# Performance work log

Hardware: AMD Instinct MI355X
Metric: run time of the kernel (lower is better)

Reference implementation:

```python
import jax, jax.numpy as jnp
import numpy as np

N = 131072
F_DIM = 128
HID = 256
POL = 512
EPS = 1e-5


def _lin(key, fan_in, fan_out):
    k1, k2 = jax.random.split(key)
    s = 1.0 / np.sqrt(fan_in)
    W = jax.random.uniform(k1, (fan_in, fan_out), jnp.float32, -s, s)
    b = jax.random.uniform(k2, (fan_out,), jnp.float32, -s, s)
    return W, b


def setup_inputs() -> dict:
    key = jax.random.key(0)
    ks = jax.random.split(key, 12)
    observation = jax.random.normal(ks[0], (N, F_DIM), jnp.float32)
    mask = jnp.ones((N, 1), jnp.float32)
    # dense_to_sparse(eye(N)) -> pure self-loop edge list
    ar = jnp.arange(N, dtype=jnp.int32)
    edge_index = jnp.stack([ar, ar])  # [2, N]
    W1, b1 = _lin(ks[1], F_DIM, HID)
    Wg, bg = _lin(ks[2], HID, HID)     # GCNConv weight/bias
    ln_w = jnp.ones((HID,), jnp.float32)
    ln_b = jnp.zeros((HID,), jnp.float32)
    Wgate, bgate = _lin(ks[3], HID, 1)
    Wd, bd = _lin(ks[4], HID, HID)
    Wp1, bp1 = _lin(ks[5], HID, POL)
    Wp2, bp2 = _lin(ks[6], POL, POL)
    Wv, bv = _lin(ks[7], POL, 1)
    return dict(observation=observation, mask=mask, edge_index=edge_index,
                W1=W1, b1=b1, Wg=Wg, bg=bg, ln_w=ln_w, ln_b=ln_b,
                Wgate=Wgate, bgate=bgate, Wd=Wd, bd=bd,
                Wp1=Wp1, bp1=bp1, Wp2=Wp2, bp2=bp2, Wv=Wv, bv=bv)


def reference(observation, mask, edge_index, W1, b1, Wg, bg, ln_w, ln_b,
              Wgate, bgate, Wd, bd, Wp1, bp1, Wp2, bp2, Wv, bv):
    n = observation.shape[0]
    # encoder_1 + relu
    X = jax.nn.relu(observation @ W1 + b1)  # [N,256]

    # GCNConv(256,256): add self-loops, symmetric norm, gather/scatter
    ar = jnp.arange(n, dtype=edge_index.dtype)
    ei = jnp.concatenate([edge_index, jnp.stack([ar, ar])], axis=1)  # [2,E+N]
    row, col = ei[0], ei[1]
    Xw = X @ Wg
    deg = jax.ops.segment_sum(jnp.ones(ei.shape[1], X.dtype), col, num_segments=n)
    dinv = jnp.where(deg > 0, jax.lax.rsqrt(deg), 0.0)
    norm = dinv[row] * dinv[col]
    msg = Xw[row] * norm[:, None]
    Xg = jax.ops.segment_sum(msg, col, num_segments=n) + bg
    Xg = jax.nn.relu(Xg)

    # PyG LayerNorm, mode='graph' (batch=None): global mean/std over all elements
    mu = Xg.mean()
    sd = jnp.sqrt(jnp.mean((Xg - mu) ** 2))  # std, unbiased=False
    Xn = (Xg - mu) / (sd + EPS) * ln_w + ln_b

    # AttentionalAggregation with sigmoid gate -> [1,256]
    gate = jax.nn.sigmoid(Xn @ Wgate + bgate)  # [N,1]
    pooled = jnp.sum(gate * Xn, axis=0, keepdims=True)

    h = jax.nn.relu(pooled @ Wd + bd)
    h = jax.nn.relu(h @ Wp1 + bp1)
    h = jax.nn.relu(h @ Wp2 + bp2)
    value = h @ Wv + bv  # [1,1]
    return value * mask  # broadcast -> [N,1]
```

## Files before the change

### kernel.cpp

```cpp
#include <hip/hip_runtime.h>

#define NROWS 131072
#define EPSV 1e-5f

typedef __attribute__((ext_vector_type(8))) short short8;
typedef __attribute__((ext_vector_type(4))) short bfx4;
typedef __attribute__((ext_vector_type(4))) float floatx4;

__device__ __forceinline__ short f2bf(float f){
  unsigned u = __builtin_bit_cast(unsigned, f);
  return (short)((u + 0x8000u) >> 16);
}
__device__ __forceinline__ float bf2f(unsigned h){
  unsigned u = h << 16;
  return __builtin_bit_cast(float, u);
}

__device__ __forceinline__ int XIDX(int row, int col){
  return row*256 + ((((col >> 3) ^ (row & 31))) << 3) + (col & 7);
}

__global__ __launch_bounds__(256) void prep_kernel(
    const float* __restrict__ W1, const float* __restrict__ Wg,
    const float* __restrict__ lnw, const float* __restrict__ lnb,
    const float* __restrict__ Wgate,
    short* __restrict__ W1s, short* __restrict__ Wgs,
    float* __restrict__ u, float* accum)
{
  const int b = blockIdx.x, tid = threadIdx.x;
  if (b < 16){
    int idx = b*256 + tid;
    int lane = idx & 63, rg = idx >> 6;
    int ctg = rg & 15, kt = rg >> 4;
    int kb = kt*32 + (lane>>4)*8;
    int c  = ctg*16 + (lane&15);
    short8 t;
    #pragma unroll
    for (int j=0;j<8;j++) t[j] = f2bf(W1[(kb+j)*256 + c]);
    *(short8*)(W1s + idx*8) = t;
  } else if (b < 48){
    int idx = (b-16)*256 + tid;
    int lane = idx & 63, rg = idx >> 6;
    int ctg = rg & 15, kt = rg >> 4;
    int kb = kt*32 + (lane>>4)*8;
    int c  = ctg*16 + (lane&15);
    short8 t;
    #pragma unroll
    for (int j=0;j<8;j++) t[j] = f2bf(Wg[(kb+j)*256 + c]);
    *(short8*)(Wgs + idx*8) = t;
  } else {
    __shared__ float red[8];
    float uv = lnw[tid] * Wgate[tid];
    float lv = lnb[tid] * Wgate[tid];
    u[tid] = uv;
    float a = uv, c = lv;
    #pragma unroll
    for (int off=32; off; off >>= 1){
      a += __shfl_down(a, off);
      c += __shfl_down(c, off);
    }
    const int w = tid >> 6, l = tid & 63;
    if (l == 0){ red[w] = a; red[4+w] = c; }
    __syncthreads();
    if (tid == 0){
      accum[4] = red[0]+red[1]+red[2]+red[3];
      accum[5] = red[4]+red[5]+red[6]+red[7];
    }
  }
}

__global__ __launch_bounds__(256, 3) void gemm12_kernel(
    const float* __restrict__ obs, const float* __restrict__ b1,
    const float* __restrict__ bg,
    const short* __restrict__ W1s, const short* __restrict__ Wgs,
    const float* __restrict__ u,
    short* __restrict__ XgT, float* __restrict__ d, float* __restrict__ pS)
{
  __shared__ short Xs[64*256];
  float* dacc = (float*)Xs;
  short* As = Xs;
  const int tid = threadIdx.x;
  const int w = tid >> 6, l = tid & 63, q = l >> 4, lm = l & 15;
  const long R = (long)blockIdx.x * 64;

  short8 bc[4], bn[4];
  float bias1[4];
  #pragma unroll
  for (int ct=0; ct<4; ct++){
    bc[ct] = *(const short8*)(W1s + (((w*4+ct))*64 + l)*8);
    bias1[ct] = b1[w*64 + ct*16 + lm];
  }

  #pragma unroll
  for (int rt=0; rt<4; rt++){
    const float* ap = obs + (R + rt*16 + lm)*128 + w*32 + q*8;
    floatx4 f0 = *(const floatx4*)ap;
    floatx4 f1 = *(const floatx4*)(ap + 4);
    short8 t;
    t[0]=f2bf(f0[0]); t[1]=f2bf(f0[1]); t[2]=f2bf(f0[2]); t[3]=f2bf(f0[3]);
    t[4]=f2bf(f1[0]); t[5]=f2bf(f1[1]); t[6]=f2bf(f1[2]); t[7]=f2bf(f1[3]);
    *(short8*)(As + ((w*4 + rt)*64 + l)*8) = t;
  }
  __syncthreads();

  floatx4 acc[4][4];
  #pragma unroll
  for (int ct=0; ct<4; ct++){
    floatx4 bi = {bias1[ct], bias1[ct], bias1[ct], bias1[ct]};
    #pragma unroll
    for (int rt=0; rt<4; rt++) acc[rt][ct] = bi;
  }

  short8 ac[4], an[4];
  #pragma unroll
  for (int rt=0; rt<4; rt++)
    ac[rt] = *(const short8*)(As + ((0*4 + rt)*64 + l)*8);
  #pragma unroll
  for (int kt=0; kt<4; kt++){
    if (kt < 3){
      #pragma unroll
      for (int ct=0; ct<4; ct++)
        bn[ct] = *(const short8*)(W1s + (((kt+1)*16 + (w*4+ct))*64 + l)*8);
      #pragma unroll
      for (int rt=0; rt<4; rt++)
        an[rt] = *(const short8*)(As + (((kt+1)*4 + rt)*64 + l)*8);
    }
    #pragma unroll
    for (int ct=0; ct<4; ct++)
      #pragma unroll
      for (int rt=0; rt<4; rt++)
        acc[rt][ct] = __builtin_amdgcn_mfma_f32_16x16x32_bf16(ac[rt], bc[ct], acc[rt][ct], 0,0,0);
    if (kt < 3){
      #pragma unroll
      for (int i=0;i<4;i++){ bc[i]=bn[i]; ac[i]=an[i]; }
    }
  }

  float bias2[4], uc[4];
  #pragma unroll
  for (int ct=0; ct<4; ct++){
    bc[ct] = *(const short8*)(Wgs + (((w*4+ct))*64 + l)*8);
    bias2[ct] = bg[w*64 + ct*16 + lm];
    uc[ct]    = u [w*64 + ct*16 + lm];
  }

  __syncthreads();

  #pragma unroll
  for (int ct=0; ct<4; ct++){
    const int col = w*64 + ct*16 + lm;
    #pragma unroll
    for (int rt=0; rt<4; rt++)
      #pragma unroll
      for (int r=0;r<4;r++)
        Xs[XIDX(rt*16 + q*4 + r, col)] = f2bf(fmaxf(acc[rt][ct][r], 0.f));
  }
  __syncthreads();

  #pragma unroll
  for (int ct=0; ct<4; ct++){
    floatx4 bi = {bias2[ct], bias2[ct], bias2[ct], bias2[ct]};
    #pragma unroll
    for (int rt=0; rt<4; rt++) acc[rt][ct] = bi;
  }
  #pragma unroll
  for (int rt=0; rt<4; rt++)
    ac[rt] = *(const short8*)(Xs + XIDX(rt*16 + lm, 0*32 + q*8));
  #pragma unroll
  for (int kt=0; kt<8; kt++){
    if (kt < 7){
      #pragma unroll
      for (int ct=0; ct<4; ct++)
        bn[ct] = *(const short8*)(Wgs + (((kt+1)*16 + (w*4+ct))*64 + l)*8);
      #pragma unroll
      for (int rt=0; rt<4; rt++)
        an[rt] = *(const short8*)(Xs + XIDX(rt*16 + lm, (kt+1)*32 + q*8));
    }
    #pragma unroll
    for (int ct=0; ct<4; ct++)
      #pragma unroll
      for (int rt=0; rt<4; rt++)
        acc[rt][ct] = __builtin_amdgcn_mfma_f32_16x16x32_bf16(ac[rt], bc[ct], acc[rt][ct], 0,0,0);
    if (kt < 7){
      #pragma unroll
      for (int i=0;i<4;i++){ bc[i]=bn[i]; ac[i]=an[i]; }
    }
  }
  __syncthreads();

  float s1 = 0.f, s2 = 0.f;
  float dp[16];
  #pragma unroll
  for (int i=0;i<16;i++) dp[i] = 0.f;
  #pragma unroll
  for (int ct=0; ct<4; ct++){
    const int col = w*64 + ct*16 + lm;
    const float uv = uc[ct];
    #pragma unroll
    for (int rt=0; rt<4; rt++){
      float v0 = fmaxf(acc[rt][ct][0], 0.f);
      float v1 = fmaxf(acc[rt][ct][1], 0.f);
      float v2 = fmaxf(acc[rt][ct][2], 0.f);
      float v3 = fmaxf(acc[rt][ct][3], 0.f);
      s1 += (v0+v1)+(v2+v3);
      s2 += v0*v0 + v1*v1 + v2*v2 + v3*v3;
      dp[rt*4+0] += v0*uv; dp[rt*4+1] += v1*uv;
      dp[rt*4+2] += v2*uv; dp[rt*4+3] += v3*uv;
      bfx4 pk = {f2bf(v0), f2bf(v1), f2bf(v2), f2bf(v3)};
      *(bfx4*)(XgT + (long)col*NROWS + R + rt*16 + q*4) = pk;
    }
  }
  #pragma unroll
  for (int rt=0; rt<4; rt++)
    #pragma unroll
    for (int r=0; r<4; r++)
      dacc[(w*64 + rt*16 + q*4 + r)*17 + lm] = dp[rt*4+r];

  #pragma unroll
  for (int off=32; off; off >>= 1){
    s1 += __shfl_down(s1, off);
    s2 += __shfl_down(s2, off);
  }
  if (l == 0){
    pS[blockIdx.x*4 + w] = s1;
    pS[8192 + blockIdx.x*4 + w] = s2;
  }
  __syncthreads();

  {
    const int row = tid >> 2, g = tid & 3;
    float s = 0.f;
    #pragma unroll
    for (int wv=0; wv<4; wv++)
      #pragma unroll
      for (int j=0; j<4; j++)
        s += dacc[(wv*64 + row)*17 + g*4 + j];
    s += __shfl_xor(s, 1);
    s += __shfl_xor(s, 2);
    if (g == 0) d[R + row] = s;
  }
}

__global__ __launch_bounds__(256) void stats_kernel(
    const float* __restrict__ pS, const float* __restrict__ bgate,
    float* __restrict__ accum)
{
  __shared__ float red[8];
  const int tid = threadIdx.x, w = tid >> 6, l = tid & 63;
  float a = 0.f, b = 0.f;
  #pragma unroll
  for (int i=0;i<32;i++){
    a += pS[tid + 256*i];
    b += pS[8192 + tid + 256*i];
  }
  #pragma unroll
  for (int off=32; off; off >>= 1){
    a += __shfl_down(a, off);
    b += __shfl_down(b, off);
  }
  if (l == 0){ red[w] = a; red[4+w] = b; }
  __syncthreads();
  if (tid == 0){
    const float NE = (float)NROWS * 256.f;
    const float S1 = red[0]+red[1]+red[2]+red[3];
    const float S2 = red[4]+red[5]+red[6]+red[7];
    const float mu = S1 / NE;
    float var = S2 / NE - mu*mu;
    var = var > 0.f ? var : 0.f;
    const float inv = 1.f / (sqrtf(var) + EPSV);
    accum[0] = inv;
    accum[1] = -inv*mu*accum[4] + accum[5] + bgate[0];
    accum[2] = mu;
  }
}

__global__ __launch_bounds__(256) void pool_kernel(
    const short* __restrict__ XgT, const float* __restrict__ dvec,
    const float* __restrict__ accum,
    float* __restrict__ gxPart, float* __restrict__ gsPart)
{
  __shared__ float spj[4][8];
  __shared__ float sgs[4];
  const int tid = threadIdx.x, w = tid >> 6, l = tid & 63;
  const float inv = accum[0];
  const float gc  = accum[1];

  const int rs = blockIdx.x >> 5, cg = blockIdx.x & 31, c0 = cg*8;
  float p[8];
  #pragma unroll
  for (int j=0;j<8;j++) p[j] = 0.f;
  float gs = 0.f;

  #pragma unroll
  for (int it=0; it<2; it++){
    const int r0 = rs*4096 + it*2048 + tid*8;
    floatx4 dv0 = *(const floatx4*)(dvec + r0);
    floatx4 dv1 = *(const floatx4*)(dvec + r0 + 4);
    float g[8];
    g[0] = 1.f/(1.f + __expf(-(inv*dv0[0] + gc)));
    g[1] = 1.f/(1.f + __expf(-(inv*dv0[1] + gc)));
    g[2] = 1.f/(1.f + __expf(-(inv*dv0[2] + gc)));
    g[3] = 1.f/(1.f + __expf(-(inv*dv0[3] + gc)));
    g[4] = 1.f/(1.f + __expf(-(inv*dv1[0] + gc)));
    g[5] = 1.f/(1.f + __expf(-(inv*dv1[1] + gc)));
    g[6] = 1.f/(1.f + __expf(-(inv*dv1[2] + gc)));
    g[7] = 1.f/(1.f + __expf(-(inv*dv1[3] + gc)));
    gs += ((g[0]+g[1])+(g[2]+g[3])) + ((g[4]+g[5])+(g[6]+g[7]));
    #pragma unroll
    for (int j=0;j<8;j++){
      short8 xv = *(const short8*)(XgT + (long)(c0+j)*NROWS + r0);
      float s = 0.f;
      #pragma unroll
      for (int k=0;k<8;k++) s += g[k]*bf2f((unsigned short)xv[k]);
      p[j] += s;
    }
  }
  #pragma unroll
  for (int j=0;j<8;j++)
    #pragma unroll
    for (int off=32; off; off >>= 1) p[j] += __shfl_down(p[j], off);
  #pragma unroll
  for (int off=32; off; off >>= 1) gs += __shfl_down(gs, off);
  if (l == 0){
    #pragma unroll
    for (int j=0;j<8;j++) spj[w][j] = p[j];
    sgs[w] = gs;
  }
  __syncthreads();
  if (tid < 8)
    gxPart[rs*256 + c0 + tid] = spj[0][tid]+spj[1][tid]+spj[2][tid]+spj[3][tid];
  if (cg == 0 && tid == 8)
    gsPart[rs] = sgs[0]+sgs[1]+sgs[2]+sgs[3];
}

__global__ __launch_bounds__(256) void mlp1_kernel(
    const float* __restrict__ lnw, const float* __restrict__ lnb,
    const float* __restrict__ Wd,  const float* __restrict__ bd,
    const float* __restrict__ accum, const float* __restrict__ gxPart,
    const float* __restrict__ gsPart, float* __restrict__ h1)
{
  __shared__ float xa[256];
  __shared__ float redG;
  __shared__ float sp[4][64];
  const int tid = threadIdx.x, w = tid >> 6, l = tid & 63;
  const float inv = accum[0];
  const float mu  = accum[2];

  if (w == 0){
    float gg = (l < 32) ? gsPart[l] : 0.f;
    #pragma unroll
    for (int off=32; off; off >>= 1) gg += __shfl_down(gg, off);
    if (l == 0) redG = gg;
  }
  __syncthreads();
  const float G = redG;

  {
    float sgx = 0.f;
    #pragma unroll
    for (int s=0;s<32;s++) sgx += gxPart[s*256 + tid];
    const float lw = lnw[tid];
    xa[tid] = inv*lw*sgx + (lnb[tid] - mu*inv*lw)*G;
  }
  __syncthreads();

  const int j = blockIdx.x*64 + l;
  const int k0 = w*64;
  const float* wp = Wd + (long)k0*256 + j;
  float p0=0.f,p1=0.f,p2=0.f,p3=0.f;
  #pragma unroll
  for (int k=0; k<64; k+=4){
    p0 += xa[k0+k  ] * wp[(k  )*256];
    p1 += xa[k0+k+1] * wp[(k+1)*256];
    p2 += xa[k0+k+2] * wp[(k+2)*256];
    p3 += xa[k0+k+3] * wp[(k+3)*256];
  }
  sp[w][l] = (p0+p1)+(p2+p3);
  __syncthreads();
  if (w == 0)
    h1[j] = fmaxf(sp[0][l]+sp[1][l]+sp[2][l]+sp[3][l] + bd[j], 0.f);
}

__global__ __launch_bounds__(256) void mlp_mid(
    const float* __restrict__ W, const float* __restrict__ bias,
    const float* __restrict__ x, float* __restrict__ y,
    const int inDim, const int outDim)
{
  __shared__ float sp[4][64];
  const int l = threadIdx.x & 63, w = threadIdx.x >> 6;
  const int j = blockIdx.x*64 + l;
  const int kq = inDim >> 2, k0 = w*kq;
  const float* wp = W + (long)k0*outDim + j;
  float p0=0.f,p1=0.f,p2=0.f,p3=0.f;
  for (int k=0; k<kq; k+=4){
    p0 += x[k0+k  ] * wp[(long)(k  )*outDim];
    p1 += x[k0+k+1] * wp[(long)(k+1)*outDim];
    p2 += x[k0+k+2] * wp[(long)(k+2)*outDim];
    p3 += x[k0+k+3] * wp[(long)(k+3)*outDim];
  }
  sp[w][l] = (p0+p1)+(p2+p3);
  __syncthreads();
  if (w == 0)
    y[j] = fmaxf(sp[0][l]+sp[1][l]+sp[2][l]+sp[3][l] + bias[j], 0.f);
}

__global__ __launch_bounds__(256) void bcast_kernel(
    const float* __restrict__ h3, const float* __restrict__ Wv,
    const float* __restrict__ bv, const float* __restrict__ mask,
    float* __restrict__ out)
{
  __shared__ float red[4];
  const int tid = threadIdx.x, w = tid >> 6, l = tid & 63;
  float p = h3[tid]*Wv[tid] + h3[tid+256]*Wv[tid+256];
  #pragma unroll
  for (int off=32; off; off >>= 1) p += __shfl_down(p, off);
  if (l == 0) red[w] = p;
  __syncthreads();
  const float value = red[0]+red[1]+red[2]+red[3] + bv[0];

  const long i = (long)blockIdx.x*256 + tid;
  floatx4 m = *(const floatx4*)(mask + i*4);
  floatx4 o = {m[0]*value, m[1]*value, m[2]*value, m[3]*value};
  *(floatx4*)(out + i*4) = o;
}

extern "C" void kernel_launch(void* const* d_in, const int* in_sizes, int n_in,
                              void* d_out, int out_size, void* d_ws, size_t ws_size,
                              hipStream_t stream)
{
  const float* obs   = (const float*)d_in[0];
  const float* mask  = (const float*)d_in[1];
  const float* W1    = (const float*)d_in[3];
  const float* b1    = (const float*)d_in[4];
  const float* Wg    = (const float*)d_in[5];
  const float* bg    = (const float*)d_in[6];
  const float* lnw   = (const float*)d_in[7];
  const float* lnb   = (const float*)d_in[8];
  const float* Wgate = (const float*)d_in[9];
  const float* bgate = (const float*)d_in[10];
  const float* Wd    = (const float*)d_in[11];
  const float* bd    = (const float*)d_in[12];
  const float* Wp1   = (const float*)d_in[13];
  const float* bp1   = (const float*)d_in[14];
  const float* Wp2   = (const float*)d_in[15];
  const float* bp2   = (const float*)d_in[16];
  const float* Wv    = (const float*)d_in[17];
  const float* bv    = (const float*)d_in[18];
  float* out = (float*)d_out;

  char* wsb = (char*)d_ws;
  short* XgT   = (short*)(wsb);
  short* W1s   = (short*)(wsb + 67108864);
  short* Wgs   = (short*)(wsb + 67174400);
  float* u     = (float*)(wsb + 67305472);
  float* dvec  = (float*)(wsb + 67306496);
  float* pS    = (float*)(wsb + 67830784);
  float* gxP   = (float*)(wsb + 67896320);
  float* gsP   = (float*)(wsb + 67929088);
  float* accum = (float*)(wsb + 67930112);
  float* h1    = (float*)(wsb + 67931136);
  float* h2    = (float*)(wsb + 67932160);
  float* h3    = (float*)(wsb + 67934208);

  prep_kernel<<<49, 256, 0, stream>>>(W1, Wg, lnw, lnb, Wgate, W1s, Wgs, u, accum);
  gemm12_kernel<<<2048, 256, 0, stream>>>(obs, b1, bg, W1s, Wgs, u, XgT, dvec, pS);
  stats_kernel<<<1, 256, 0, stream>>>(pS, bgate, accum);
  pool_kernel<<<1024, 256, 0, stream>>>(XgT, dvec, accum, gxP, gsP);
  mlp1_kernel<<<4, 256, 0, stream>>>(lnw, lnb, Wd, bd, accum, gxP, gsP, h1);
  mlp_mid<<<8, 256, 0, stream>>>(Wp1, bp1, h1, h2, 256, 512);
  mlp_mid<<<8, 256, 0, stream>>>(Wp2, bp2, h2, h3, 512, 512);
  bcast_kernel<<<128, 256, 0, stream>>>(h3, Wv, bv, mask, out);
}
```

Measured before the change: 221.5 us.

## Fuse stats into GEMM via last-block counter and merge MLP tail kernels

The separate stats kernel is removed. The last gemm12 block to finish, found with an atomic counter and threadfence, now reduces the partial sums and writes the normalization constants. The four small MLP and broadcast kernels are merged into one tail kernel of 16 blocks, and each block recomputes the whole MLP before writing its slice of the output. This removes several launch and inter-kernel gaps, at the cost of redundant MLP work in each block and a serialized reduction at the end of the GEMM.

```diff
diff --git a/kernel.cpp b/kernel.cpp
--- a/kernel.cpp
+++ b/kernel.cpp
@@ -25,7 +25,7 @@
     const float* __restrict__ lnw, const float* __restrict__ lnb,
     const float* __restrict__ Wgate,
     short* __restrict__ W1s, short* __restrict__ Wgs,
-    float* __restrict__ u, float* accum)
+    float* __restrict__ u, float* accum, unsigned* __restrict__ counter)
 {
   const int b = blockIdx.x, tid = threadIdx.x;
   if (b < 16){
@@ -65,6 +65,7 @@
     if (tid == 0){
       accum[4] = red[0]+red[1]+red[2]+red[3];
       accum[5] = red[4]+red[5]+red[6]+red[7];
+      counter[0] = 0u;
     }
   }
 }
@@ -73,10 +74,12 @@
     const float* __restrict__ obs, const float* __restrict__ b1,
     const float* __restrict__ bg,
     const short* __restrict__ W1s, const short* __restrict__ Wgs,
-    const float* __restrict__ u,
-    short* __restrict__ XgT, float* __restrict__ d, float* __restrict__ pS)
+    const float* __restrict__ u, const float* __restrict__ bgate,
+    short* __restrict__ XgT, float* __restrict__ d, float* __restrict__ pS,
+    float* __restrict__ accum, unsigned* __restrict__ counter)
 {
   __shared__ short Xs[64*256];
+  __shared__ unsigned tick;
   float* dacc = (float*)Xs;
   short* As = Xs;
   const int tid = threadIdx.x;
@@ -239,38 +242,38 @@
     s += __shfl_xor(s, 2);
     if (g == 0) d[R + row] = s;
   }
-}
-
-__global__ __launch_bounds__(256) void stats_kernel(
-    const float* __restrict__ pS, const float* __restrict__ bgate,
-    float* __restrict__ accum)
-{
-  __shared__ float red[8];
-  const int tid = threadIdx.x, w = tid >> 6, l = tid & 63;
-  float a = 0.f, b = 0.f;
-  #pragma unroll
-  for (int i=0;i<32;i++){
-    a += pS[tid + 256*i];
-    b += pS[8192 + tid + 256*i];
-  }
-  #pragma unroll
-  for (int off=32; off; off >>= 1){
-    a += __shfl_down(a, off);
-    b += __shfl_down(b, off);
-  }
-  if (l == 0){ red[w] = a; red[4+w] = b; }
-  __syncthreads();
-  if (tid == 0){
-    const float NE = (float)NROWS * 256.f;
-    const float S1 = red[0]+red[1]+red[2]+red[3];
-    const float S2 = red[4]+red[5]+red[6]+red[7];
-    const float mu = S1 / NE;
-    float var = S2 / NE - mu*mu;
-    var = var > 0.f ? var : 0.f;
-    const float inv = 1.f / (sqrtf(var) + EPSV);
-    accum[0] = inv;
-    accum[1] = -inv*mu*accum[4] + accum[5] + bgate[0];
-    accum[2] = mu;
+
+  __threadfence();
+  __syncthreads();
+  if (tid == 0) tick = atomicAdd(counter, 1u);
+  __syncthreads();
+  if (tick == 2047u){
+    __threadfence();
+    float a = 0.f, b = 0.f;
+    #pragma unroll
+    for (int i=0;i<32;i++){
+      a += pS[tid + 256*i];
+      b += pS[8192 + tid + 256*i];
+    }
+    #pragma unroll
+    for (int off=32; off; off >>= 1){
+      a += __shfl_down(a, off);
+      b += __shfl_down(b, off);
+    }
+    if (l == 0){ dacc[w] = a; dacc[4+w] = b; }
+    __syncthreads();
+    if (tid == 0){
+      const float NE = (float)NROWS * 256.f;
+      const float S1 = dacc[0]+dacc[1]+dacc[2]+dacc[3];
+      const float S2 = dacc[4]+dacc[5]+dacc[6]+dacc[7];
+      const float mu = S1 / NE;
+      float var = S2 / NE - mu*mu;
+      var = var > 0.f ? var : 0.f;
+      const float inv = 1.f / (sqrtf(var) + EPSV);
+      accum[0] = inv;
+      accum[1] = -inv*mu*accum[4] + accum[5] + bgate[0];
+      accum[2] = mu;
+    }
   }
 }
 
@@ -333,18 +336,22 @@
     gsPart[rs] = sgs[0]+sgs[1]+sgs[2]+sgs[3];
 }
 
-__global__ __launch_bounds__(256) void mlp1_kernel(
+__global__ __launch_bounds__(256) void tail_kernel(
     const float* __restrict__ lnw, const float* __restrict__ lnb,
     const float* __restrict__ Wd,  const float* __restrict__ bd,
+    const float* __restrict__ Wp1, const float* __restrict__ bp1,
+    const float* __restrict__ Wp2, const float* __restrict__ bp2,
+    const float* __restrict__ Wv,  const float* __restrict__ bv,
     const float* __restrict__ accum, const float* __restrict__ gxPart,
-    const float* __restrict__ gsPart, float* __restrict__ h1)
+    const float* __restrict__ gsPart, const float* __restrict__ mask,
+    float* __restrict__ out)
 {
-  __shared__ float xa[256];
+  __shared__ float xa[256], v1[256], v2[512], v3[512];
+  __shared__ float sp[2048];
+  __shared__ float redv[4];
   __shared__ float redG;
-  __shared__ float sp[4][64];
   const int tid = threadIdx.x, w = tid >> 6, l = tid & 63;
-  const float inv = accum[0];
-  const float mu  = accum[2];
+  const float inv = accum[0], mu = accum[2];
 
   if (w == 0){
     float gg = (l < 32) ? gsPart[l] : 0.f;
@@ -352,76 +359,96 @@
     for (int off=32; off; off >>= 1) gg += __shfl_down(gg, off);
     if (l == 0) redG = gg;
   }
-  __syncthreads();
-  const float G = redG;
-
-  {
-    float sgx = 0.f;
-    #pragma unroll
-    for (int s=0;s<32;s++) sgx += gxPart[s*256 + tid];
-    const float lw = lnw[tid];
+  float sgx = 0.f;
+  #pragma unroll
+  for (int s=0;s<32;s++) sgx += gxPart[s*256 + tid];
+  __syncthreads();
+  {
+    const float G = redG, lw = lnw[tid];
     xa[tid] = inv*lw*sgx + (lnb[tid] - mu*inv*lw)*G;
   }
   __syncthreads();
 
-  const int j = blockIdx.x*64 + l;
-  const int k0 = w*64;
-  const float* wp = Wd + (long)k0*256 + j;
-  float p0=0.f,p1=0.f,p2=0.f,p3=0.f;
-  #pragma unroll
-  for (int k=0; k<64; k+=4){
-    p0 += xa[k0+k  ] * wp[(k  )*256];
-    p1 += xa[k0+k+1] * wp[(k+1)*256];
-    p2 += xa[k0+k+2] * wp[(k+2)*256];
-    p3 += xa[k0+k+3] * wp[(k+3)*256];
-  }
-  sp[w][l] = (p0+p1)+(p2+p3);
-  __syncthreads();
-  if (w == 0)
-    h1[j] = fmaxf(sp[0][l]+sp[1][l]+sp[2][l]+sp[3][l] + bd[j], 0.f);
-}
-
-__global__ __launch_bounds__(256) void mlp_mid(
-    const float* __restrict__ W, const float* __restrict__ bias,
-    const float* __restrict__ x, float* __restrict__ y,
-    const int inDim, const int outDim)
-{
-  __shared__ float sp[4][64];
-  const int l = threadIdx.x & 63, w = threadIdx.x >> 6;
-  const int j = blockIdx.x*64 + l;
-  const int kq = inDim >> 2, k0 = w*kq;
-  const float* wp = W + (long)k0*outDim + j;
-  float p0=0.f,p1=0.f,p2=0.f,p3=0.f;
-  for (int k=0; k<kq; k+=4){
-    p0 += x[k0+k  ] * wp[(long)(k  )*outDim];
-    p1 += x[k0+k+1] * wp[(long)(k+1)*outDim];
-    p2 += x[k0+k+2] * wp[(long)(k+2)*outDim];
-    p3 += x[k0+k+3] * wp[(long)(k+3)*outDim];
-  }
-  sp[w][l] = (p0+p1)+(p2+p3);
-  __syncthreads();
-  if (w == 0)
-    y[j] = fmaxf(sp[0][l]+sp[1][l]+sp[2][l]+sp[3][l] + bias[j], 0.f);
-}
-
-__global__ __launch_bounds__(256) void bcast_kernel(
-    const float* __restrict__ h3, const float* __restrict__ Wv,
-    const float* __restrict__ bv, const float* __restrict__ mask,
-    float* __restrict__ out)
-{
-  __shared__ float red[4];
-  const int tid = threadIdx.x, w = tid >> 6, l = tid & 63;
-  float p = h3[tid]*Wv[tid] + h3[tid+256]*Wv[tid+256];
-  #pragma unroll
-  for (int off=32; off; off >>= 1) p += __shfl_down(p, off);
-  if (l == 0) red[w] = p;
-  __syncthreads();
-  const float value = red[0]+red[1]+red[2]+red[3] + bv[0];
-
-  const long i = (long)blockIdx.x*256 + tid;
-  floatx4 m = *(const floatx4*)(mask + i*4);
-  floatx4 o = {m[0]*value, m[1]*value, m[2]*value, m[3]*value};
-  *(floatx4*)(out + i*4) = o;
+  {
+    const int k0 = w*64;
+    const float* wp = Wd + (long)k0*256;
+    float a0=0.f,a1=0.f,a2=0.f,a3=0.f;
+    #pragma unroll 4
+    for (int k=0;k<64;k++){
+      const float x = xa[k0+k];
+      a0 += x*wp[k*256 + l];
+      a1 += x*wp[k*256 + 64 + l];
+      a2 += x*wp[k*256 + 128 + l];
+      a3 += x*wp[k*256 + 192 + l];
+    }
+    sp[w*256 + l]       = a0; sp[w*256 + 64 + l]  = a1;
+    sp[w*256 + 128 + l] = a2; sp[w*256 + 192 + l] = a3;
+  }
+  __syncthreads();
+  v1[tid] = fmaxf(sp[tid]+sp[256+tid]+sp[512+tid]+sp[768+tid] + bd[tid], 0.f);
+  __syncthreads();
+
+  {
+    const int k0 = w*64;
+    const float* wp = Wp1 + (long)k0*512;
+    float a[8];
+    #pragma unroll
+    for (int m=0;m<8;m++) a[m] = 0.f;
+    #pragma unroll 2
+    for (int k=0;k<64;k++){
+      const float x = v1[k0+k];
+      #pragma unroll
+      for (int m=0;m<8;m++) a[m] += x*wp[k*512 + m*64 + l];
+    }
+    #pragma unroll
+    for (int m=0;m<8;m++) sp[w*512 + m*64 + l] = a[m];
+  }
+  __syncthreads();
+  v2[tid]     = fmaxf(sp[tid]    +sp[512+tid]    +sp[1024+tid]    +sp[1536+tid]
+                      + bp1[tid], 0.f);
+  v2[256+tid] = fmaxf(sp[256+tid]+sp[768+tid]    +sp[1280+tid]    +sp[1792+tid]
+                      + bp1[256+tid], 0.f);
+  __syncthreads();
+
+  {
+    const int k0 = w*128;
+    const float* wp = Wp2 + (long)k0*512;
+    float a[8];
+    #pragma unroll
+    for (int m=0;m<8;m++) a[m] = 0.f;
+    #pragma unroll 2
+    for (int k=0;k<128;k++){
+      const float x = v2[k0+k];
+      #pragma unroll
+      for (int m=0;m<8;m++) a[m] += x*wp[k*512 + m*64 + l];
+    }
+    #pragma unroll
+    for (int m=0;m<8;m++) sp[w*512 + m*64 + l] = a[m];
+  }
+  __syncthreads();
+  v3[tid]     = fmaxf(sp[tid]    +sp[512+tid]    +sp[1024+tid]    +sp[1536+tid]
+                      + bp2[tid], 0.f);
+  v3[256+tid] = fmaxf(sp[256+tid]+sp[768+tid]    +sp[1280+tid]    +sp[1792+tid]
+                      + bp2[256+tid], 0.f);
+  __syncthreads();
+
+  {
+    float p = v3[tid]*Wv[tid] + v3[256+tid]*Wv[256+tid];
+    #pragma unroll
+    for (int off=32; off; off >>= 1) p += __shfl_down(p, off);
+    if (l == 0) redv[w] = p;
+  }
+  __syncthreads();
+  const float value = redv[0]+redv[1]+redv[2]+redv[3] + bv[0];
+
+  const long base = (long)blockIdx.x*8192;
+  #pragma unroll
+  for (int it=0; it<8; it++){
+    const long i = base + it*1024 + tid*4;
+    floatx4 m4 = *(const floatx4*)(mask + i);
+    floatx4 o = {m4[0]*value, m4[1]*value, m4[2]*value, m4[3]*value};
+    *(floatx4*)(out + i) = o;
+  }
 }
 
 extern "C" void kernel_launch(void* const* d_in, const int* in_sizes, int n_in,
@@ -458,16 +485,13 @@
   float* gxP   = (float*)(wsb + 67896320);
   float* gsP   = (float*)(wsb + 67929088);
   float* accum = (float*)(wsb + 67930112);
-  float* h1    = (float*)(wsb + 67931136);
-  float* h2    = (float*)(wsb + 67932160);
-  float* h3    = (float*)(wsb + 67934208);
-
-  prep_kernel<<<49, 256, 0, stream>>>(W1, Wg, lnw, lnb, Wgate, W1s, Wgs, u, accum);
-  gemm12_kernel<<<2048, 256, 0, stream>>>(obs, b1, bg, W1s, Wgs, u, XgT, dvec, pS);
-  stats_kernel<<<1, 256, 0, stream>>>(pS, bgate, accum);
+  unsigned* counter = (unsigned*)(wsb + 67930112 + 256);
+
+  prep_kernel<<<49, 256, 0, stream>>>(W1, Wg, lnw, lnb, Wgate, W1s, Wgs, u,
+                                      accum, counter);
+  gemm12_kernel<<<2048, 256, 0, stream>>>(obs, b1, bg, W1s, Wgs, u, bgate,
+                                          XgT, dvec, pS, accum, counter);
   pool_kernel<<<1024, 256, 0, stream>>>(XgT, dvec, accum, gxP, gsP);
-  mlp1_kernel<<<4, 256, 0, stream>>>(lnw, lnb, Wd, bd, accum, gxP, gsP, h1);
-  mlp_mid<<<8, 256, 0, stream>>>(Wp1, bp1, h1, h2, 256, 512);
-  mlp_mid<<<8, 256, 0, stream>>>(Wp2, bp2, h2, h3, 512, 512);
-  bcast_kernel<<<128, 256, 0, stream>>>(h3, Wv, bv, mask, out);
-}
+  tail_kernel<<<16, 256, 0, stream>>>(lnw, lnb, Wd, bd, Wp1, bp1, Wp2, bp2,
+                                      Wv, bv, accum, gxP, gsP, mask, out);
+}
```

Result: slower. 541.9 us (+144.6%).
